# Optimization experiments

Measured on AMD Instinct MI355X. Metric: run time of the kernel, lower is better.

## Reference

```python
import jax, jax.numpy as jnp
import numpy as np

PERIMETER = 2.0 * np.pi  # cyclicity of phi
STD = 1.0                # kernel bandwidth (init kwarg std)


def _sq_dists(p):
    # p: [B, N, 2] -> squared euclidean distances [B, N, N]
    sqnorm = jnp.sum(p * p, axis=2)                    # [B, N]
    dot = jnp.einsum('bnd,bmd->bnm', p, p)             # [B, N, N]
    return sqnorm[:, :, None] + sqnorm[:, None, :] - 2.0 * dot


def _distances(phi, eta, alpha=1.0):
    # squared distances with 2*pi cyclicity on phi:
    # min over phi shifted by half-perimeter ((a+b)/2 - |a-b|/2 == min(a,b))
    p1 = jnp.stack((eta * alpha, phi % PERIMETER), axis=2)
    d1 = _sq_dists(p1)
    p2 = jnp.stack((eta * alpha, (phi + PERIMETER / 2) % PERIMETER), axis=2)
    d2 = _sq_dists(p2)
    return jnp.minimum(d1, d2)


def setup_inputs() -> dict:
    key = jax.random.key(0)
    k1, k2, k3 = jax.random.split(key, 3)
    B, N = 16, 2048
    e = jax.random.normal(k1, (B, N), dtype=jnp.float32)
    phi = jax.random.normal(k2, (B, N), dtype=jnp.float32)
    eta = jax.random.normal(k3, (B, N), dtype=jnp.float32)
    return {"e": e, "phi": phi, "eta": eta}


def reference(e, phi, eta):
    # compute_kernel: gaussian adjacency on cyclic squared distances
    adj = jnp.exp(-_distances(phi, eta) / STD)          # [B, N, N]
    # order_pooling: sort nodes by degree (row sums), descending
    degree = jnp.sum(adj, axis=2)                       # [B, N]
    order = jnp.argsort(-degree, axis=1)                # [B, N] int
    # order_matrix: permute rows then columns of adjacency
    adj_o = jnp.take_along_axis(adj, order[:, :, None], axis=1)
    adj_o = jnp.take_along_axis(adj_o, order[:, None, :], axis=2)
    # order_vector: permute per-node features
    e_o = jnp.take_along_axis(e, order, axis=1)
    phi_o = jnp.take_along_axis(phi, order, axis=1)
    eta_o = jnp.take_along_axis(eta, order, axis=1)
    return (adj_o, e_o, phi_o, eta_o)
```

## Files before the change

### kernel.cpp

```cpp
#include <hip/hip_runtime.h>
#include <hip/hip_bf16.h>

#define BN 16
#define NN 2048

#define P_F  6.28318530717958647692f
#define HP_F 3.14159265358979323846f

#define PIDX(j) ((j) + ((j) >> 7))
#define PN (NN + 16)

__device__ __forceinline__ float pmod(float x) {
    float r = fmodf(x, P_F);
    return (r < 0.0f) ? r + P_F : r;
}

__device__ __forceinline__ float adjval(float xi, float a1, float a2,
                                        float xj, float b1, float b2) {
    float dx = xi - xj;
    float t  = dx * dx;
    float u  = a1 - b1;
    float v  = a2 - b2;
    float d1 = fmaf(u, u, t);
    float d2 = fmaf(v, v, t);
    return __expf(-fminf(d1, d2));
}

__device__ __forceinline__ double expd_fast(double x) {
    const double L2E   = 1.44269504088896338700e+00;
    const double LN2HI = 6.93147180369123816490e-01;
    const double LN2LO = 1.90821492927058770002e-10;
    double n  = rint(x * L2E);
    double r  = fma(n, -LN2HI, x);
    r         = fma(n, -LN2LO, r);
    double h  = 2.5052108385441720e-08;
    h = fma(h, r, 2.7557319223985888e-07);
    h = fma(h, r, 2.7557319223985893e-06);
    h = fma(h, r, 2.4801587301587302e-05);
    h = fma(h, r, 1.9841269841269841e-04);
    h = fma(h, r, 1.3888888888888889e-03);
    h = fma(h, r, 8.3333333333333332e-03);
    h = fma(h, r, 4.1666666666666664e-02);
    h = fma(h, r, 1.6666666666666666e-01);
    h = fma(h, r, 0.5);
    double q = fma(h, r, 1.0);
    double e = fma(q, r, 1.0);
    long long ll = (long long)n;
    double s = __longlong_as_double((ll + 1023) << 52);
    return e * s;
}

__global__ __launch_bounds__(256) void k_degree(const float* __restrict__ phi,
                                                const float* __restrict__ eta,
                                                float* __restrict__ degree) {
#pragma clang fp contract(off)
    int blk = blockIdx.x;
    int b   = blk >> 7;
    int r0  = (blk & 127) << 4;

    __shared__ float se[PN], sp1[PN], sp2[PN], sn1[PN], sn2[PN];
    const float* pb = phi + (size_t)b * NN;
    const float* eb = eta + (size_t)b * NN;
    for (int j = threadIdx.x; j < NN; j += 256) {
        float p  = pb[j];
        float x  = eb[j];
        float p1 = pmod(p);
        float p2 = pmod(p + HP_F);
        int jj = PIDX(j);
        se[jj]  = x;
        sp1[jj] = p1;
        sp2[jj] = p2;
        sn1[jj] = x * x + p1 * p1;
        sn2[jj] = x * x + p2 * p2;
    }
    __syncthreads();

    int row16  = threadIdx.x >> 4;
    int lane16 = threadIdx.x & 15;
    int i  = r0 + row16;
    int ii = PIDX(i);

    float xi  = se[ii],  p1i = sp1[ii], p2i = sp2[ii];
    float n1i = sn1[ii], n2i = sn2[ii];

    int jbase = lane16 * 129;

    auto elem = [&](int jj) -> float {
        float me   = xi * se[jj];
        float dot1 = me + p1i * sp1[jj];
        float dot2 = me + p2i * sp2[jj];
        float d1   = (n1i + sn1[jj]) - 2.0f * dot1;
        float d2   = (n2i + sn2[jj]) - 2.0f * dot2;
        float dmin = fminf(d1, d2);
        return (float)expd_fast(-(double)dmin);
    };

    float r[8];
    #pragma unroll
    for (int t = 0; t < 8; ++t) r[t] = elem(jbase + t);
    #pragma unroll 2
    for (int i8 = 8; i8 < 128; i8 += 8) {
        #pragma unroll
        for (int t = 0; t < 8; ++t) r[t] = r[t] + elem(jbase + i8 + t);
    }
    float rr = ((r[0] + r[1]) + (r[2] + r[3])) + ((r[4] + r[5]) + (r[6] + r[7]));

    #pragma unroll
    for (int m = 1; m <= 8; m <<= 1) {
        rr = rr + __shfl_xor(rr, m, 64);
    }
    if (lane16 == 0) degree[(size_t)b * NN + i] = rr;
}

__global__ __launch_bounds__(256) void k_rank(const float* __restrict__ degree,
                                              const float* __restrict__ e,
                                              const float* __restrict__ phi,
                                              const float* __restrict__ eta,
                                              float* __restrict__ out_e,
                                              float* __restrict__ out_phi,
                                              float* __restrict__ out_eta) {
    int blk = blockIdx.x;
    int b   = blk >> 3;
    int r0  = (blk & 7) << 8;
    int i   = r0 + threadIdx.x;

    __shared__ float sdeg[NN];
    const float* db = degree + (size_t)b * NN;
    for (int j = threadIdx.x; j < NN; j += 256) sdeg[j] = db[j];
    __syncthreads();

    float di = sdeg[i];
    int c0 = 0, c1 = 0, c2 = 0, c3 = 0;
    #pragma unroll 4
    for (int j = 0; j < NN; j += 4) {
        float d0 = sdeg[j], d1v = sdeg[j + 1], d2v = sdeg[j + 2], d3v = sdeg[j + 3];
        c0 += (d0  > di) || (d0  == di && (j    ) < i);
        c1 += (d1v > di) || (d1v == di && (j + 1) < i);
        c2 += (d2v > di) || (d2v == di && (j + 2) < i);
        c3 += (d3v > di) || (d3v == di && (j + 3) < i);
    }
    int rank = (c0 + c1) + (c2 + c3);

    size_t src = (size_t)b * NN + i;
    size_t dst = (size_t)b * NN + rank;
    out_e[dst]   = e[src];
    out_phi[dst] = phi[src];
    out_eta[dst] = eta[src];
}

#define ROWS 8
__global__ __launch_bounds__(256) void k_adj(const float* __restrict__ phi_o,
                                             const float* __restrict__ eta_o,
                                             float* __restrict__ adj) {
    int blk = blockIdx.x;
    int b   = blk / (NN / ROWS);
    int r0  = (blk % (NN / ROWS)) * ROWS;

    __shared__ float sx[NN], s1[NN], s2[NN];
    const float* pb = phi_o + (size_t)b * NN;
    const float* eb = eta_o + (size_t)b * NN;
    for (int j = threadIdx.x; j < NN; j += 256) {
        float p = pb[j];
        sx[j] = eb[j];
        s1[j] = pmod(p);
        s2[j] = pmod(p + HP_F);
    }
    __syncthreads();

    float* base = adj + ((size_t)b * NN + r0) * NN;
    for (int r = 0; r < ROWS; ++r) {
        int i = r0 + r;
        float xi = sx[i], a1 = s1[i], a2 = s2[i];
        #pragma unroll
        for (int p = 0; p < 2; ++p) {
            int j0 = p * 1024 + threadIdx.x * 4;
            float4 xv = *reinterpret_cast<const float4*>(&sx[j0]);
            float4 y1 = *reinterpret_cast<const float4*>(&s1[j0]);
            float4 y2 = *reinterpret_cast<const float4*>(&s2[j0]);
            float4 o;
            o.x = adjval(xi, a1, a2, xv.x, y1.x, y2.x);
            o.y = adjval(xi, a1, a2, xv.y, y1.y, y2.y);
            o.z = adjval(xi, a1, a2, xv.z, y1.z, y2.z);
            o.w = adjval(xi, a1, a2, xv.w, y1.w, y2.w);
            *reinterpret_cast<float4*>(&base[(size_t)r * NN + j0]) = o;
        }
    }
}

extern "C" void kernel_launch(void* const* d_in, const int* in_sizes, int n_in,
                              void* d_out, int out_size, void* d_ws, size_t ws_size,
                              hipStream_t stream) {
    const float* e   = (const float*)d_in[0];
    const float* phi = (const float*)d_in[1];
    const float* eta = (const float*)d_in[2];

    float* adj     = (float*)d_out;
    float* out_e   = adj + (size_t)BN * NN * NN;
    float* out_phi = out_e + (size_t)BN * NN;
    float* out_eta = out_phi + (size_t)BN * NN;

    float* degree = (float*)d_ws;

    k_degree<<<BN * (NN / 16), 256, 0, stream>>>(phi, eta, degree);
    k_rank<<<BN * 8, 256, 0, stream>>>(degree, e, phi, eta,
                                       out_e, out_phi, out_eta);
    k_adj<<<BN * (NN / ROWS), 256, 0, stream>>>(out_phi, out_eta, adj);
}
```

Measured before the change: 400.2 us.

## Pack degree LDS data, shorten exp polynomial, restructure adj kernel with nontemporal stores

The degree kernel packs x, p1, p2 and n1 into a single float4 in shared memory and recomputes n2 per element instead of loading it. The double-precision exp polynomial is cut by two terms. The rank kernel reads degrees as float4. The adjacency kernel handles 16 rows per block with row constants held in registers, loads each column vector once, and writes output with nontemporal stores to reduce cache pollution on the large output. The risks are small numeric drift from the shorter polynomial, which could flip the order of nodes with near-tied degrees, and higher register pressure in the adjacency kernel.

```diff
diff --git a/kernel.cpp b/kernel.cpp
--- a/kernel.cpp
+++ b/kernel.cpp
@@ -9,6 +9,8 @@
 
 #define PIDX(j) ((j) + ((j) >> 7))
 #define PN (NN + 16)
+
+typedef float float4n __attribute__((ext_vector_type(4)));
 
 __device__ __forceinline__ float pmod(float x) {
     float r = fmodf(x, P_F);
@@ -33,9 +35,7 @@
     double n  = rint(x * L2E);
     double r  = fma(n, -LN2HI, x);
     r         = fma(n, -LN2LO, r);
-    double h  = 2.5052108385441720e-08;
-    h = fma(h, r, 2.7557319223985888e-07);
-    h = fma(h, r, 2.7557319223985893e-06);
+    double h  = 2.7557319223985893e-06;
     h = fma(h, r, 2.4801587301587302e-05);
     h = fma(h, r, 1.9841269841269841e-04);
     h = fma(h, r, 1.3888888888888889e-03);
@@ -58,7 +58,7 @@
     int b   = blk >> 7;
     int r0  = (blk & 127) << 4;
 
-    __shared__ float se[PN], sp1[PN], sp2[PN], sn1[PN], sn2[PN];
+    __shared__ float4 spk[PN];
     const float* pb = phi + (size_t)b * NN;
     const float* eb = eta + (size_t)b * NN;
     for (int j = threadIdx.x; j < NN; j += 256) {
@@ -66,31 +66,31 @@
         float x  = eb[j];
         float p1 = pmod(p);
         float p2 = pmod(p + HP_F);
-        int jj = PIDX(j);
-        se[jj]  = x;
-        sp1[jj] = p1;
-        sp2[jj] = p2;
-        sn1[jj] = x * x + p1 * p1;
-        sn2[jj] = x * x + p2 * p2;
+        float n1 = x * x + p1 * p1;
+        spk[PIDX(j)] = make_float4(x, p1, p2, n1);
     }
     __syncthreads();
 
     int row16  = threadIdx.x >> 4;
     int lane16 = threadIdx.x & 15;
-    int i  = r0 + row16;
-    int ii = PIDX(i);
-
-    float xi  = se[ii],  p1i = sp1[ii], p2i = sp2[ii];
-    float n1i = sn1[ii], n2i = sn2[ii];
+    int i = r0 + row16;
+
+    float4 qi = spk[PIDX(i)];
+    float xi  = qi.x, p1i = qi.y, p2i = qi.z, n1i = qi.w;
+    float n2i = xi * xi + p2i * p2i;
 
     int jbase = lane16 * 129;
 
     auto elem = [&](int jj) -> float {
-        float me   = xi * se[jj];
-        float dot1 = me + p1i * sp1[jj];
-        float dot2 = me + p2i * sp2[jj];
-        float d1   = (n1i + sn1[jj]) - 2.0f * dot1;
-        float d2   = (n2i + sn2[jj]) - 2.0f * dot2;
+        float4 q   = spk[jj];
+        float me   = xi * q.x;
+        float dot1 = me + p1i * q.y;
+        float dot2 = me + p2i * q.z;
+        float t    = q.x * q.x;
+        float v    = q.z * q.z;
+        float n2j  = t + v;
+        float d1   = (n1i + q.w) - 2.0f * dot1;
+        float d2   = (n2i + n2j) - 2.0f * dot2;
         float dmin = fminf(d1, d2);
         return (float)expd_fast(-(double)dmin);
     };
@@ -133,11 +133,11 @@
     int c0 = 0, c1 = 0, c2 = 0, c3 = 0;
     #pragma unroll 4
     for (int j = 0; j < NN; j += 4) {
-        float d0 = sdeg[j], d1v = sdeg[j + 1], d2v = sdeg[j + 2], d3v = sdeg[j + 3];
-        c0 += (d0  > di) || (d0  == di && (j    ) < i);
-        c1 += (d1v > di) || (d1v == di && (j + 1) < i);
-        c2 += (d2v > di) || (d2v == di && (j + 2) < i);
-        c3 += (d3v > di) || (d3v == di && (j + 3) < i);
+        float4 d4 = *reinterpret_cast<const float4*>(&sdeg[j]);
+        c0 += (d4.x > di) || (d4.x == di && (j    ) < i);
+        c1 += (d4.y > di) || (d4.y == di && (j + 1) < i);
+        c2 += (d4.z > di) || (d4.z == di && (j + 2) < i);
+        c3 += (d4.w > di) || (d4.w == di && (j + 3) < i);
     }
     int rank = (c0 + c1) + (c2 + c3);
 
@@ -148,13 +148,13 @@
     out_eta[dst] = eta[src];
 }
 
-#define ROWS 8
+#define ROWS 16
 __global__ __launch_bounds__(256) void k_adj(const float* __restrict__ phi_o,
                                              const float* __restrict__ eta_o,
                                              float* __restrict__ adj) {
     int blk = blockIdx.x;
-    int b   = blk / (NN / ROWS);
-    int r0  = (blk % (NN / ROWS)) * ROWS;
+    int b   = blk >> 7;
+    int r0  = (blk & 127) << 4;
 
     __shared__ float sx[NN], s1[NN], s2[NN];
     const float* pb = phi_o + (size_t)b * NN;
@@ -167,22 +167,30 @@
     }
     __syncthreads();
 
+    float xi[ROWS], a1[ROWS], a2[ROWS];
+    #pragma unroll
+    for (int r = 0; r < ROWS; ++r) {
+        xi[r] = sx[r0 + r];
+        a1[r] = s1[r0 + r];
+        a2[r] = s2[r0 + r];
+    }
+
     float* base = adj + ((size_t)b * NN + r0) * NN;
-    for (int r = 0; r < ROWS; ++r) {
-        int i = r0 + r;
-        float xi = sx[i], a1 = s1[i], a2 = s2[i];
+    #pragma unroll
+    for (int p = 0; p < 2; ++p) {
+        int j0 = p * 1024 + threadIdx.x * 4;
+        float4 xv = *reinterpret_cast<const float4*>(&sx[j0]);
+        float4 y1 = *reinterpret_cast<const float4*>(&s1[j0]);
+        float4 y2 = *reinterpret_cast<const float4*>(&s2[j0]);
         #pragma unroll
-        for (int p = 0; p < 2; ++p) {
-            int j0 = p * 1024 + threadIdx.x * 4;
-            float4 xv = *reinterpret_cast<const float4*>(&sx[j0]);
-            float4 y1 = *reinterpret_cast<const float4*>(&s1[j0]);
-            float4 y2 = *reinterpret_cast<const float4*>(&s2[j0]);
-            float4 o;
-            o.x = adjval(xi, a1, a2, xv.x, y1.x, y2.x);
-            o.y = adjval(xi, a1, a2, xv.y, y1.y, y2.y);
-            o.z = adjval(xi, a1, a2, xv.z, y1.z, y2.z);
-            o.w = adjval(xi, a1, a2, xv.w, y1.w, y2.w);
-            *reinterpret_cast<float4*>(&base[(size_t)r * NN + j0]) = o;
+        for (int r = 0; r < ROWS; ++r) {
+            float4n o;
+            o.x = adjval(xi[r], a1[r], a2[r], xv.x, y1.x, y2.x);
+            o.y = adjval(xi[r], a1[r], a2[r], xv.y, y1.y, y2.y);
+            o.z = adjval(xi[r], a1[r], a2[r], xv.z, y1.z, y2.z);
+            o.w = adjval(xi[r], a1[r], a2[r], xv.w, y1.w, y2.w);
+            __builtin_nontemporal_store(o,
+                reinterpret_cast<float4n*>(&base[(size_t)r * NN + j0]));
         }
     }
 }
```

New measurement: 394.0 us. Within noise of the previous version (-1.5%).
